# Optimization experiments

Measured on AMD Instinct MI355X. Metric: run time of the kernel, lower is better.

Reference implementation:

```python
import jax, jax.numpy as jnp
import numpy as np

HEAD_SIZE = 64

def setup_inputs() -> dict:
    key = jax.random.key(0)
    k1, k2, k3, k4 = jax.random.split(key, 4)
    B, T, C = 4, 4096, 768
    s = 1.0 / np.sqrt(C)
    return {
        "x": jax.random.normal(k1, (B, T, C), dtype=jnp.float32),
        "Wq": jax.random.normal(k2, (C, HEAD_SIZE), dtype=jnp.float32) * s,
        "Wk": jax.random.normal(k3, (C, HEAD_SIZE), dtype=jnp.float32) * s,
        "Wv": jax.random.normal(k4, (C, HEAD_SIZE), dtype=jnp.float32) * s,
    }

def reference(x, Wq, Wk, Wv):
    # x: [B,T,C]; Wq/Wk/Wv: [C,H]
    T = x.shape[1]
    q = jnp.einsum('btc,ch->bth', x, Wq)
    k = jnp.einsum('btc,ch->bth', x, Wk)
    v = jnp.einsum('btc,ch->bth', x, Wv)
    scale = HEAD_SIZE ** (-0.5)
    wei = jnp.einsum('bth,bsh->bts', q, k) * scale  # [B,T,T]
    causal = jnp.tril(jnp.ones((T, T), dtype=bool))
    wei = jnp.where(causal, wei, -jnp.inf)
    wei = jax.nn.softmax(wei, axis=-1)
    # dropout p=0.0 -> identity
    out = jnp.einsum('bts,bsh->bth', wei, v)  # [B,T,H]
    return out
```

## Files before the change

kernel.cpp:

```cpp
#include <hip/hip_runtime.h>
#include <hip/hip_bf16.h>
#include <stdint.h>
#include <math.h>

typedef unsigned short u16;
typedef __attribute__((ext_vector_type(8))) __bf16 bf16x8;
typedef __attribute__((ext_vector_type(4))) float f32x4;

#define LOG2E 1.44269504088896340736f

__device__ inline u16 f2bf(float f){
  uint32_t u = __float_as_uint(f);
  u += 0x7FFFu + ((u >> 16) & 1u);
  return (u16)(u >> 16);
}
__device__ inline float bf2f(u16 v){
  return __uint_as_float(((uint32_t)v) << 16);
}

__global__ __launch_bounds__(256) void wt_kernel(const float* __restrict__ Wq,
                                                 const float* __restrict__ Wk,
                                                 const float* __restrict__ Wv,
                                                 u16* __restrict__ wtf){
  int idx = blockIdx.x * 256 + threadIdx.x;
  if (idx >= 192 * 768) return;
  int n = idx / 768, c = idx - n * 768;
  int h = n & 63;
  const float* W = (n < 64) ? Wq : ((n < 128) ? Wk : Wv);
  float v = W[c * 64 + h];
  if (n < 64) v *= 0.125f * LOG2E;
  int f = n >> 4, n16 = n & 15;
  int kstep = c >> 5, quad = (c >> 3) & 3, j = c & 7;
  wtf[(size_t)((f * 24 + kstep) * 64 + quad * 16 + n16) * 8 + j] = f2bf(v);
}

__global__ __launch_bounds__(256) void proj_kernel(const float* __restrict__ x,
                                                   const u16* __restrict__ wtf,
                                                   u16* __restrict__ qs,
                                                   u16* __restrict__ ksf,
                                                   u16* __restrict__ vtf){
  __shared__ u16 At[24 * 64 * 8];
  const int tid = threadIdx.x;
  const int w = tid >> 6, lane = tid & 63;
  const int n16 = lane & 15, quad = lane >> 4;
  const int rt = blockIdx.x * 16;
  const float* xb = x + (size_t)rt * 768;

  float4 tr0, tr1, tr2;
#define LOADR(c) {                                                           \
    int jj0 = tid,       r0 = jj0 / 48, q0 = jj0 - r0 * 48;                  \
    int jj1 = 256 + tid, r1 = jj1 / 48, q1 = jj1 - r1 * 48;                  \
    int jj2 = 512 + tid, r2 = jj2 / 48, q2 = jj2 - r2 * 48;                  \
    tr0 = *(const float4*)(xb + ((size_t)r0 * 192 + (c) * 48 + q0) * 4);     \
    tr1 = *(const float4*)(xb + ((size_t)r1 * 192 + (c) * 48 + q1) * 4);     \
    tr2 = *(const float4*)(xb + ((size_t)r2 * 192 + (c) * 48 + q2) * 4);     \
  }
#define WR1(c, jj, t) {                                                      \
    int rr = (jj) / 48, ql = (jj) - rr * 48;                                 \
    int ksn = (c) * 6 + (ql >> 3), qd = (ql >> 1) & 3, j0 = (ql & 1) * 4;    \
    int idx = ((ksn * 64 + qd * 16 + rr) * 8 + j0) ^ ((ksn & 7) << 3);       \
    union { ushort4 s; u16 e[4]; } pk;                                       \
    pk.e[0] = f2bf(t.x); pk.e[1] = f2bf(t.y);                                \
    pk.e[2] = f2bf(t.z); pk.e[3] = f2bf(t.w);                                \
    *(ushort4*)&At[idx] = pk.s;                                              \
  }
#define WRITES(c) { WR1(c, tid, tr0); WR1(c, 256 + tid, tr1); WR1(c, 512 + tid, tr2); }
#define COMPUTE(c) {                                                         \
    _Pragma("unroll") for (int kk = 0; kk < 6; ++kk){                        \
      int kst = (c) * 6 + kk;                                                \
      int sw = (kst & 7) << 3;                                               \
      bf16x8 a = *(const bf16x8*)&At[((kst * 64 + lane) * 8) ^ sw];          \
      _Pragma("unroll") for (int j = 0; j < 3; ++j){                         \
        bf16x8 bfr = *(const bf16x8*)(wtf + (size_t)(((3 * w + j) * 24 + kst) * 64 + lane) * 8); \
        acc[j] = __builtin_amdgcn_mfma_f32_16x16x32_bf16(a, bfr, acc[j], 0, 0, 0); \
      }                                                                      \
    }                                                                        \
  }

  const f32x4 fz = {0.f, 0.f, 0.f, 0.f};
  f32x4 acc[3];
#pragma unroll
  for (int j = 0; j < 3; ++j) acc[j] = fz;

  const int ch0 = blockIdx.x & 3;
  const int ch1 = (ch0 + 1) & 3, ch2 = (ch0 + 2) & 3, ch3 = (ch0 + 3) & 3;

  LOADR(ch0); WRITES(ch0);
  __syncthreads();
  LOADR(ch1);
  COMPUTE(ch0);
  WRITES(ch1);
  __syncthreads();
  LOADR(ch2);
  COMPUTE(ch1);
  WRITES(ch2);
  __syncthreads();
  LOADR(ch3);
  COMPUTE(ch2);
  WRITES(ch3);
  __syncthreads();
  COMPUTE(ch3);
  __syncthreads();
#undef LOADR
#undef WR1
#undef WRITES
#undef COMPUTE

#pragma unroll
  for (int j = 0; j < 3; ++j){
    const int F = 3 * w + j;
    const int s = F >> 2, c0 = (F & 3) * 16;
#pragma unroll
    for (int r = 0; r < 4; ++r){
      u16 val = f2bf(acc[j][r]);
      int row = quad * 4 + r;
      if (s < 2) At[s * 1152 + row * 72 + c0 + n16] = val;
      else       At[2304 + (c0 + n16) * 24 + row]   = val;
    }
  }
  __syncthreads();

  const int bb = rt >> 12, t0 = rt & 4095;
  const int kt = t0 >> 6;
  const int fk = (t0 >> 4) & 3;
  const int half0 = (t0 >> 5) & 1;
  const int qhalf = (t0 >> 4) & 1;
  if (tid < 128){
    int row = tid >> 3, hc = tid & 7;
    uint4 qv = *(const uint4*)&At[row * 72 + hc * 8];
    *(uint4*)(qs + (size_t)(rt + row) * 64 + hc * 8) = qv;
  } else {
    int tt = tid - 128;
    int half = tt >> 6, l2 = tt & 63;
    int nn = l2 & 15, qq = l2 >> 4;
    uint4 kv = *(const uint4*)&At[1152 + nn * 72 + half * 32 + qq * 8];
    size_t off = ((((size_t)(bb * 64 + kt) * 4 + fk) * 2 + half) * 64 + l2) * 8;
    *(uint4*)(ksf + off) = kv;
  }
  if (tid < 128){
    int f = tid >> 5, idx5 = tid & 31;
    int qsel = idx5 >> 4, nn = idx5 & 15;
    int h = f * 16 + nn;
    uint4 vv = *(const uint4*)&At[2304 + h * 24 + qsel * 8];
    int lane2 = (2 * qhalf + qsel) * 16 + nn;
    size_t off = ((((size_t)(bb * 64 + kt) * 4 + f) * 2 + half0) * 64 + lane2) * 8;
    *(uint4*)(vtf + off) = vv;
  }
}

__global__ __launch_bounds__(256) void flash_part(const u16* __restrict__ qs,
                                                  const u16* __restrict__ ksf,
                                                  const u16* __restrict__ vtf,
                                                  u16* __restrict__ Opart,
                                                  float* __restrict__ ml){
  const int gid = blockIdx.x;
  int b, qt, ck, nt;
  if (gid < 1024){
    b = gid >> 8;
    int r = gid & 255;
    int m = (int)sqrtf((float)r);
    if (m * m > r) --m;
    if ((m + 1) * (m + 1) <= r) ++m;
    int d = r - m * m;
    if (d < m){ qt = 2 * m;     ck = d;     }
    else      { qt = 2 * m + 1; ck = d - m; }
    nt = 4;
  } else {
    int t = gid - 1024;
    b = t >> 4;
    int m = t & 15;
    qt = 2 * m; ck = m; nt = 2;
  }
  const int kt0 = ck * 4;

  __shared__ u16 Kb[4096];
  __shared__ u16 Vb[4096];
  __shared__ u16 Ps[128 * 72];
  const int tid = threadIdx.x;
  const int w = tid >> 6, lane = tid & 63;
  const int n16 = lane & 15, quad = lane >> 4;

  const u16* qb  = qs  + (size_t)b * 262144;
  const u16* kpg = ksf + (size_t)b * 262144 + (size_t)kt0 * 4096;
  const u16* vpg = vtf + (size_t)b * 262144 + (size_t)kt0 * 4096;

  bf16x8 qA[2][2];
#pragma unroll
  for (int m = 0; m < 2; ++m){
    const size_t qrow = (size_t)(qt * 128 + w * 32 + m * 16 + n16) * 64;
    qA[m][0] = *(const bf16x8*)(qb + qrow + quad * 8);
    qA[m][1] = *(const bf16x8*)(qb + qrow + 32 + quad * 8);
  }

  const f32x4 fz = {0.f, 0.f, 0.f, 0.f};
  f32x4 O[2][4];
  float rs[2][4];
#pragma unroll
  for (int m = 0; m < 2; ++m)
#pragma unroll
    for (int f = 0; f < 4; ++f){ O[m][f] = fz; rs[m][f] = 0.f; }

  uint4 rk0, rk1, rv0, rv1;
#define LOADR(ti)                                                            \
  {                                                                          \
    const u16* kg = kpg + (size_t)(ti) * 4096 + tid * 16;                    \
    const u16* vg = vpg + (size_t)(ti) * 4096 + tid * 16;                    \
    rk0 = *(const uint4*)kg;  rk1 = *(const uint4*)(kg + 8);                 \
    rv0 = *(const uint4*)vg;  rv1 = *(const uint4*)(vg + 8);                 \
  }
#define WRITES()                                                             \
  {                                                                          \
    *(uint4*)&Kb[tid * 16] = rk0;  *(uint4*)&Kb[tid * 16 + 8] = rk1;         \
    *(uint4*)&Vb[tid * 16] = rv0;  *(uint4*)&Vb[tid * 16 + 8] = rv1;         \
  }

  LOADR(0);
  WRITES();
  __syncthreads();

  for (int it = 0; it < nt; ++it){
    const int kt = kt0 + it;
    if (it + 1 < nt) LOADR(it + 1);

    f32x4 S[2][4];
#pragma unroll
    for (int f = 0; f < 4; ++f){
      bf16x8 k0 = *(const bf16x8*)&Kb[(f * 2 + 0) * 512 + lane * 8];
      bf16x8 k1 = *(const bf16x8*)&Kb[(f * 2 + 1) * 512 + lane * 8];
#pragma unroll
      for (int m = 0; m < 2; ++m){
        f32x4 s = fz;
        s = __builtin_amdgcn_mfma_f32_16x16x32_bf16(qA[m][0], k0, s, 0, 0, 0);
        s = __builtin_amdgcn_mfma_f32_16x16x32_bf16(qA[m][1], k1, s, 0, 0, 0);
        S[m][f] = s;
      }
    }

    if (kt >= 2 * qt){
#pragma unroll
      for (int m = 0; m < 2; ++m)
#pragma unroll
        for (int f = 0; f < 4; ++f)
#pragma unroll
          for (int r = 0; r < 4; ++r){
            int col = kt * 64 + f * 16 + n16;
            int row = qt * 128 + w * 32 + m * 16 + quad * 4 + r;
            if (col > row) S[m][f][r] = -1e30f;
          }
    }

#pragma unroll
    for (int m = 0; m < 2; ++m)
#pragma unroll
      for (int f = 0; f < 4; ++f)
#pragma unroll
        for (int r = 0; r < 4; ++r){
          float p = __builtin_amdgcn_exp2f(S[m][f][r]);
          S[m][f][r] = p;
          rs[m][r] += p;
        }

#pragma unroll
    for (int m = 0; m < 2; ++m)
#pragma unroll
      for (int f = 0; f < 4; ++f){
        u16* p = &Ps[(w * 32 + m * 16 + quad * 4) * 72 + f * 16 + n16];
        p[0]   = f2bf(S[m][f][0]);
        p[72]  = f2bf(S[m][f][1]);
        p[144] = f2bf(S[m][f][2]);
        p[216] = f2bf(S[m][f][3]);
      }
    bf16x8 pA[2][2];
#pragma unroll
    for (int m = 0; m < 2; ++m){
      pA[m][0] = *(const bf16x8*)&Ps[(w * 32 + m * 16 + n16) * 72 + quad * 8];
      pA[m][1] = *(const bf16x8*)&Ps[(w * 32 + m * 16 + n16) * 72 + 32 + quad * 8];
    }

#pragma unroll
    for (int f = 0; f < 4; ++f){
      bf16x8 v0 = *(const bf16x8*)&Vb[(f * 2 + 0) * 512 + lane * 8];
      bf16x8 v1 = *(const bf16x8*)&Vb[(f * 2 + 1) * 512 + lane * 8];
#pragma unroll
      for (int m = 0; m < 2; ++m){
        O[m][f] = __builtin_amdgcn_mfma_f32_16x16x32_bf16(pA[m][0], v0, O[m][f], 0, 0, 0);
        O[m][f] = __builtin_amdgcn_mfma_f32_16x16x32_bf16(pA[m][1], v1, O[m][f], 0, 0, 0);
      }
    }

    if (it + 1 < nt){
      __syncthreads();
      WRITES();
      __syncthreads();
    }
  }
#undef LOADR
#undef WRITES

#pragma unroll
  for (int m = 0; m < 2; ++m)
#pragma unroll
    for (int r = 0; r < 4; ++r){
#pragma unroll
      for (int off = 1; off < 16; off <<= 1)
        rs[m][r] += __shfl_xor(rs[m][r], off, 16);
    }

  const size_t oidx = (size_t)gid * 8192;
#pragma unroll
  for (int m = 0; m < 2; ++m)
#pragma unroll
    for (int f = 0; f < 4; ++f)
#pragma unroll
      for (int r = 0; r < 4; ++r){
        int row_local = w * 32 + m * 16 + quad * 4 + r;
        Opart[oidx + (size_t)row_local * 64 + f * 16 + n16] = f2bf(O[m][f][r]);
      }
  if (n16 == 0){
    float* lp = ml + (size_t)gid * 128;
#pragma unroll
    for (int m = 0; m < 2; ++m)
#pragma unroll
      for (int r = 0; r < 4; ++r)
        lp[w * 32 + m * 16 + quad * 4 + r] = rs[m][r];
  }
}

__global__ __launch_bounds__(256) void combine_kernel(const u16* __restrict__ Opart,
                                                      const float* __restrict__ ml,
                                                      float* __restrict__ out){
  const int gid = blockIdx.x * 256 + threadIdx.x;
  const int bq = gid >> 11;
  const int rem = (gid & 2047) * 4;
  const int row = rem >> 6;
  const int b = bq >> 5, qt = bq & 31;
  const int m = qt >> 1;
  const int nc4 = (qt & 1) ? (m + 1) : m;
  const int F = (qt & 1) ? (m * m + m) : (m * m);

  float L = 0.f;
  float a0 = 0.f, a1 = 0.f, a2 = 0.f, a3 = 0.f;
  for (int j = 0; j < nc4; ++j){
    int p = b * 256 + F + j;
    L += ml[(size_t)p * 128 + row];
    const u16* q = Opart + (size_t)p * 8192 + rem;
    uint2 d = *(const uint2*)q;
    a0 += bf2f((u16)(d.x & 0xffffu));
    a1 += bf2f((u16)(d.x >> 16));
    a2 += bf2f((u16)(d.y & 0xffffu));
    a3 += bf2f((u16)(d.y >> 16));
  }
  if (!(qt & 1)){
    int p = 1024 + b * 16 + m;
    L += ml[(size_t)p * 128 + row];
    const u16* q = Opart + (size_t)p * 8192 + rem;
    uint2 d = *(const uint2*)q;
    a0 += bf2f((u16)(d.x & 0xffffu));
    a1 += bf2f((u16)(d.x >> 16));
    a2 += bf2f((u16)(d.y & 0xffffu));
    a3 += bf2f((u16)(d.y >> 16));
  }
  const float invL = 1.0f / L;
  float4 v = {a0 * invL, a1 * invL, a2 * invL, a3 * invL};
  *(float4*)(out + (size_t)gid * 4) = v;
}

extern "C" void kernel_launch(void* const* d_in, const int* in_sizes, int n_in,
                              void* d_out, int out_size, void* d_ws, size_t ws_size,
                              hipStream_t stream){
  const float* x  = (const float*)d_in[0];
  const float* Wq = (const float*)d_in[1];
  const float* Wk = (const float*)d_in[2];
  const float* Wv = (const float*)d_in[3];
  float* out = (float*)d_out;

  u16* qs  = (u16*)d_ws;
  u16* ksf = qs  + (size_t)16384 * 64;
  u16* vtf = ksf + (size_t)16384 * 64;
  u16* wtf = vtf + (size_t)16384 * 64;
  u16* Opart = wtf + (size_t)192 * 768;
  float* ml = (float*)(Opart + (size_t)1088 * 8192);

  wt_kernel<<<576, 256, 0, stream>>>(Wq, Wk, Wv, wtf);
  proj_kernel<<<1024, 256, 0, stream>>>(x, wtf, qs, ksf, vtf);
  flash_part<<<1088, 256, 0, stream>>>(qs, ksf, vtf, Opart, ml);
  combine_kernel<<<1024, 256, 0, stream>>>(Opart, ml, out);
}
```

Measured before the change: 128.9 us.

## Fuse split-K combine into flash kernel via last-block atomic counter

Removes the separate combine kernel. Each flash_part block increments a per-(batch, q-tile) atomic counter after writing its partial output, and the last block to arrive reduces all partials for that tile and writes the final normalized output. Counters are zeroed in wt_kernel. This saves a kernel launch and the gap between kernels, but adds fences and atomics, and puts the reduction work onto a few tail blocks.

```diff
diff --git a/kernel.cpp b/kernel.cpp
--- a/kernel.cpp
+++ b/kernel.cpp
@@ -21,7 +21,9 @@
 __global__ __launch_bounds__(256) void wt_kernel(const float* __restrict__ Wq,
                                                  const float* __restrict__ Wk,
                                                  const float* __restrict__ Wv,
-                                                 u16* __restrict__ wtf){
+                                                 u16* __restrict__ wtf,
+                                                 int* __restrict__ tick){
+  if (blockIdx.x == 0 && threadIdx.x < 128) tick[threadIdx.x] = 0;
   int idx = blockIdx.x * 256 + threadIdx.x;
   if (idx >= 192 * 768) return;
   int n = idx / 768, c = idx - n * 768;
@@ -152,7 +154,9 @@
                                                   const u16* __restrict__ ksf,
                                                   const u16* __restrict__ vtf,
                                                   u16* __restrict__ Opart,
-                                                  float* __restrict__ ml){
+                                                  float* __restrict__ ml,
+                                                  float* __restrict__ out,
+                                                  int* __restrict__ tick){
   const int gid = blockIdx.x;
   int b, qt, ck, nt;
   if (gid < 1024){
@@ -176,6 +180,7 @@
   __shared__ u16 Kb[4096];
   __shared__ u16 Vb[4096];
   __shared__ u16 Ps[128 * 72];
+  __shared__ int lastflag;
   const int tid = threadIdx.x;
   const int w = tid >> 6, lane = tid & 63;
   const int n16 = lane & 15, quad = lane >> 4;
@@ -324,45 +329,49 @@
       for (int r = 0; r < 4; ++r)
         lp[w * 32 + m * 16 + quad * 4 + r] = rs[m][r];
   }
-}
-
-__global__ __launch_bounds__(256) void combine_kernel(const u16* __restrict__ Opart,
-                                                      const float* __restrict__ ml,
-                                                      float* __restrict__ out){
-  const int gid = blockIdx.x * 256 + threadIdx.x;
-  const int bq = gid >> 11;
-  const int rem = (gid & 2047) * 4;
-  const int row = rem >> 6;
-  const int b = bq >> 5, qt = bq & 31;
-  const int m = qt >> 1;
-  const int nc4 = (qt & 1) ? (m + 1) : m;
-  const int F = (qt & 1) ? (m * m + m) : (m * m);
-
-  float L = 0.f;
-  float a0 = 0.f, a1 = 0.f, a2 = 0.f, a3 = 0.f;
-  for (int j = 0; j < nc4; ++j){
-    int p = b * 256 + F + j;
-    L += ml[(size_t)p * 128 + row];
-    const u16* q = Opart + (size_t)p * 8192 + rem;
-    uint2 d = *(const uint2*)q;
-    a0 += bf2f((u16)(d.x & 0xffffu));
-    a1 += bf2f((u16)(d.x >> 16));
-    a2 += bf2f((u16)(d.y & 0xffffu));
-    a3 += bf2f((u16)(d.y >> 16));
-  }
-  if (!(qt & 1)){
-    int p = 1024 + b * 16 + m;
-    L += ml[(size_t)p * 128 + row];
-    const u16* q = Opart + (size_t)p * 8192 + rem;
-    uint2 d = *(const uint2*)q;
-    a0 += bf2f((u16)(d.x & 0xffffu));
-    a1 += bf2f((u16)(d.x >> 16));
-    a2 += bf2f((u16)(d.y & 0xffffu));
-    a3 += bf2f((u16)(d.y >> 16));
-  }
-  const float invL = 1.0f / L;
-  float4 v = {a0 * invL, a1 * invL, a2 * invL, a3 * invL};
-  *(float4*)(out + (size_t)gid * 4) = v;
+
+  const int mq = qt >> 1;
+  const int nc4 = (qt & 1) ? (mq + 1) : mq;
+  const int Fq = (qt & 1) ? (mq * mq + mq) : (mq * mq);
+  const int total = nc4 + ((qt & 1) ? 0 : 1);
+  const int bq = b * 32 + qt;
+
+  __threadfence();
+  if (tid == 0)
+    lastflag = (atomicAdd(&tick[bq], 1) == total - 1);
+  __syncthreads();
+  if (!lastflag) return;
+  __threadfence();
+
+#pragma unroll
+  for (int u = 0; u < 8; ++u){
+    const int e = (u * 256 + tid) * 4;
+    const int row = e >> 6;
+    float L = 0.f, a0 = 0.f, a1 = 0.f, a2 = 0.f, a3 = 0.f;
+    for (int j = 0; j < nc4; ++j){
+      int p = b * 256 + Fq + j;
+      L += ml[(size_t)p * 128 + row];
+      const u16* q = Opart + (size_t)p * 8192 + e;
+      uint2 d = *(const uint2*)q;
+      a0 += bf2f((u16)(d.x & 0xffffu));
+      a1 += bf2f((u16)(d.x >> 16));
+      a2 += bf2f((u16)(d.y & 0xffffu));
+      a3 += bf2f((u16)(d.y >> 16));
+    }
+    if (!(qt & 1)){
+      int p = 1024 + b * 16 + mq;
+      L += ml[(size_t)p * 128 + row];
+      const u16* q = Opart + (size_t)p * 8192 + e;
+      uint2 d = *(const uint2*)q;
+      a0 += bf2f((u16)(d.x & 0xffffu));
+      a1 += bf2f((u16)(d.x >> 16));
+      a2 += bf2f((u16)(d.y & 0xffffu));
+      a3 += bf2f((u16)(d.y >> 16));
+    }
+    const float invL = 1.0f / L;
+    float4 v = {a0 * invL, a1 * invL, a2 * invL, a3 * invL};
+    *(float4*)(out + (size_t)bq * 8192 + e) = v;
+  }
 }
 
 extern "C" void kernel_launch(void* const* d_in, const int* in_sizes, int n_in,
@@ -380,9 +389,9 @@
   u16* wtf = vtf + (size_t)16384 * 64;
   u16* Opart = wtf + (size_t)192 * 768;
   float* ml = (float*)(Opart + (size_t)1088 * 8192);
-
-  wt_kernel<<<576, 256, 0, stream>>>(Wq, Wk, Wv, wtf);
+  int* tick = (int*)(ml + (size_t)1088 * 128);
+
+  wt_kernel<<<576, 256, 0, stream>>>(Wq, Wk, Wv, wtf, tick);
   proj_kernel<<<1024, 256, 0, stream>>>(x, wtf, qs, ksf, vtf);
-  flash_part<<<1088, 256, 0, stream>>>(qs, ksf, vtf, Opart, ml);
-  combine_kernel<<<1024, 256, 0, stream>>>(Opart, ml, out);
-}
+  flash_part<<<1088, 256, 0, stream>>>(qs, ksf, vtf, Opart, ml, out, tick);
+}
```

Measured after the change: 338.4 us. 162% more time.
